# Optimization experiments

Hardware: AMD Instinct MI355X
Metric: run time of the kernel (lower is better)

## Reference

```python
import jax, jax.numpy as jnp
import numpy as np
from jax import lax

N_PER_GRAPH = 1024
B_GRAPHS = 64
AVG_DEG = 16
IN_DIM = 128
HID = 128


def setup_inputs() -> dict:
    key = jax.random.key(0)
    ks = jax.random.split(key, 16)
    N = B_GRAPHS * N_PER_GRAPH
    E = N * AVG_DEG
    rng = np.random.default_rng(0)
    g = rng.integers(0, B_GRAPHS, size=E)
    src = g * N_PER_GRAPH + rng.integers(0, N_PER_GRAPH, size=E)
    dst = g * N_PER_GRAPH + rng.integers(0, N_PER_GRAPH, size=E)
    edge_index = jnp.asarray(np.stack([src, dst]), dtype=jnp.int32)
    batch = jnp.asarray(np.arange(N) // N_PER_GRAPH, dtype=jnp.int32)

    def glorot(k, fi, fo):
        return jax.random.normal(k, (fi, fo), jnp.float32) * (1.0 / np.sqrt(fi))

    return {
        "x": jax.random.normal(ks[0], (N, IN_DIM), jnp.float32),
        "edge_index": edge_index,
        "batch": batch,
        "W1": glorot(ks[1], IN_DIM, HID), "b1": jnp.zeros((HID,), jnp.float32),
        "pw1": jax.random.normal(ks[2], (HID,), jnp.float32),
        "W2": glorot(ks[3], HID, HID // 2), "b2": jnp.zeros((HID // 2,), jnp.float32),
        "pw2": jax.random.normal(ks[4], (HID // 2,), jnp.float32),
        "W3": glorot(ks[5], HID // 2, HID // 4), "b3": jnp.zeros((HID // 4,), jnp.float32),
        "pw3": jax.random.normal(ks[6], (HID // 4,), jnp.float32),
        "W4": glorot(ks[7], HID // 4, HID // 8), "b4": jnp.zeros((HID // 8,), jnp.float32),
        "linW": glorot(ks[8], HID // 8, 1), "linb": jnp.zeros((1,), jnp.float32),
    }


def gcn_conv(x, W, b, src, dst, emask):
    N = x.shape[0]
    h = x @ W                                   # [N, out]
    m = emask.astype(x.dtype)                   # [E]
    deg = jnp.ones((N,), x.dtype).at[dst].add(m)  # in-degree incl. self loop
    dis = lax.rsqrt(deg)
    coef = dis[src] * dis[dst] * m              # [E]
    agg = jnp.zeros_like(h).at[dst].add(h[src] * coef[:, None])
    return agg + h * (dis * dis)[:, None] + b   # self-loop norm = deg^-1


def topk_pool(x, pw, src, dst, emask, n):
    # PyG TopKPooling (ratio=0.5): score = tanh(x.w/||w||); keep top n//2 per graph.
    N = x.shape[0]
    B = N // n
    k = n // 2
    score = jnp.tanh((x @ pw) / jnp.linalg.norm(pw))          # [N]
    vals, idx = lax.top_k(score.reshape(B, n), k)             # per-graph top-k
    perm = (idx + jnp.arange(B)[:, None] * n).reshape(-1)     # global kept ids
    x_new = x[perm] * vals.reshape(-1, 1)
    new_id = jnp.full((N,), -1, jnp.int32).at[perm].set(jnp.arange(B * k, dtype=jnp.int32))
    ns, nd = new_id[src], new_id[dst]
    em = emask & (ns >= 0) & (nd >= 0)
    return x_new, jnp.where(em, ns, 0), jnp.where(em, nd, 0), em, k


def reference(x, edge_index, batch, W1, b1, pw1, W2, b2, pw2, W3, b3, pw3, W4, b4, linW, linb):
    src, dst = edge_index[0], edge_index[1]
    emask = jnp.ones(src.shape, bool)
    n = N_PER_GRAPH
    act = jax.nn.relu

    x = act(gcn_conv(x, W1, b1, src, dst, emask))
    x, src, dst, emask, n = topk_pool(x, pw1, src, dst, emask, n)
    x = act(gcn_conv(x, W2, b2, src, dst, emask))
    x, src, dst, emask, n = topk_pool(x, pw2, src, dst, emask, n)
    x = act(gcn_conv(x, W3, b3, src, dst, emask))
    x, src, dst, emask, n = topk_pool(x, pw3, src, dst, emask, n)
    x = act(gcn_conv(x, W4, b4, src, dst, emask))
    # global mean pool per graph (equal-sized graphs -> reshape mean)
    B = x.shape[0] // n
    xg = x.reshape(B, n, -1).mean(axis=1)                     # [B, HID//8]
    out = (xg @ linW + linb)[:, 0] * 100.0                    # [B]
    return out
```

## Files before the change

### kernel.cpp

```cpp
#include <hip/hip_runtime.h>
#include <cstdint>
#include <cstddef>

#define CAP 64
#define EC  20480
static constexpr int BG = 64;

__global__ __launch_bounds__(256) void k_scatter(const int* __restrict__ src,
                                                 const int* __restrict__ dst,
                                                 int* __restrict__ gcur,
                                                 int2* __restrict__ ebuf) {
    __shared__ int lcnt[64], lbase[64], lpos[64];
    int tid = threadIdx.x;
    if (tid < 64) { lcnt[tid] = 0; lpos[tid] = 0; }
    __syncthreads();
    int e0 = (int)blockIdx.x * 1024;
    int ss[4], dd[4], gg[4];
    #pragma unroll
    for (int i = 0; i < 4; ++i) {
        int e = e0 + i * 256 + tid;
        ss[i] = src[e]; dd[i] = dst[e];
        gg[i] = dd[i] >> 10;
        atomicAdd(&lcnt[gg[i]], 1);
    }
    __syncthreads();
    if (tid < 64) lbase[tid] = atomicAdd(&gcur[tid], lcnt[tid]);
    __syncthreads();
    #pragma unroll
    for (int i = 0; i < 4; ++i) {
        int p = atomicAdd(&lpos[gg[i]], 1);
        int pos = lbase[gg[i]] + p;
        if (pos < EC) ebuf[(size_t)gg[i] * EC + pos] = make_int2(ss[i], dd[i]);
    }
}

__global__ __launch_bounds__(1024) void k_build(const int2* __restrict__ ebuf,
                                                const int* __restrict__ gcur,
                                                int* __restrict__ cnt,
                                                float* __restrict__ dis,
                                                int* __restrict__ slots) {
    __shared__ int lc[1024];
    int g = (int)blockIdx.x, tid = (int)threadIdx.x;
    lc[tid] = 0;
    __syncthreads();
    int ec = gcur[g]; if (ec > EC) ec = EC;
    const int2* eb = &ebuf[(size_t)g * EC];
    for (int e = tid; e < ec; e += 1024) {
        int2 sd = eb[e];
        int d = sd.y & 1023;
        int pos = atomicAdd(&lc[d], 1);
        if (pos < CAP) slots[(size_t)(g * 1024 + d) * CAP + pos] = sd.x;
    }
    __syncthreads();
    int c = lc[tid];
    cnt[g * 1024 + tid] = c;
    dis[g * 1024 + tid] = rsqrtf((float)(c + 1));
}

template<int K, int OUT>
__global__ __launch_bounds__(512) void k_gemm2(const float* __restrict__ x,
                                               const float* __restrict__ W,
                                               float* __restrict__ h, int N) {
    constexpr int KT = 32;
    constexpr int RB = 128;
    constexpr int CC = OUT / 64;
    constexpr int NW4 = (KT * OUT / 4) / 512;
    __shared__ float Ws[KT * OUT];
    __shared__ float xs[KT * RB];
    int tid = (int)threadIdx.x;
    int tx = tid & 15;
    int ty = tid >> 4;
    int row0 = (int)blockIdx.x * RB;
    const float4* W4 = (const float4*)W;

    float acc[4][CC * 4];
    #pragma unroll
    for (int r = 0; r < 4; ++r)
        #pragma unroll
        for (int c = 0; c < CC * 4; ++c) acc[r][c] = 0.f;

    int xr  = tid & 127;
    int xcb = tid >> 7;

    for (int kt = 0; kt < K; kt += KT) {
        #pragma unroll
        for (int i = 0; i < NW4; ++i) {
            int idx = tid + i * 512;
            ((float4*)Ws)[idx] = W4[(size_t)kt * (OUT / 4) + idx];
        }
        const float4* xrow = (const float4*)(x + (size_t)(row0 + xr) * K + kt);
        #pragma unroll
        for (int i = 0; i < 2; ++i) {
            int c8 = xcb * 2 + i;
            float4 v = xrow[c8];
            xs[(c8 * 4 + 0) * RB + xr] = v.x;
            xs[(c8 * 4 + 1) * RB + xr] = v.y;
            xs[(c8 * 4 + 2) * RB + xr] = v.z;
            xs[(c8 * 4 + 3) * RB + xr] = v.w;
        }
        __syncthreads();
        #pragma unroll 8
        for (int k = 0; k < KT; ++k) {
            float4 av = *(const float4*)&xs[k * RB + 4 * ty];
            float4 b0 = *(const float4*)&Ws[k * OUT + 4 * tx];
            float a_[4] = {av.x, av.y, av.z, av.w};
            float b_[4] = {b0.x, b0.y, b0.z, b0.w};
            #pragma unroll
            for (int r = 0; r < 4; ++r)
                #pragma unroll
                for (int c = 0; c < 4; ++c)
                    acc[r][c] += a_[r] * b_[c];
            if constexpr (CC == 2) {
                float4 b1 = *(const float4*)&Ws[k * OUT + 64 + 4 * tx];
                float b2_[4] = {b1.x, b1.y, b1.z, b1.w};
                #pragma unroll
                for (int r = 0; r < 4; ++r)
                    #pragma unroll
                    for (int c = 0; c < 4; ++c)
                        acc[r][4 + c] += a_[r] * b2_[c];
            }
        }
        __syncthreads();
    }
    float4* h4 = (float4*)h;
    #pragma unroll
    for (int rr = 0; rr < 4; ++rr) {
        int row = row0 + 4 * ty + rr;
        float4 o0;
        o0.x = acc[rr][0]; o0.y = acc[rr][1]; o0.z = acc[rr][2]; o0.w = acc[rr][3];
        h4[(size_t)row * (OUT / 4) + tx] = o0;
        if constexpr (CC == 2) {
            float4 o1;
            o1.x = acc[rr][4]; o1.y = acc[rr][5]; o1.z = acc[rr][6]; o1.w = acc[rr][7];
            h4[(size_t)row * (OUT / 4) + 16 + tx] = o1;
        }
    }
}

template<int K, int OUT>
__global__ __launch_bounds__(256) void k_gemm(const float* __restrict__ x,
                                              const float* __restrict__ W,
                                              float* __restrict__ h, int N) {
    constexpr int ROWS = 64;
    constexpr int KT   = (K >= 64) ? 64 : K;
    constexpr int CT   = OUT / 4;
    constexpr int RT   = 256 / CT;
    constexpr int RPT  = ROWS / RT;
    constexpr int XP   = ROWS + 4;
    __shared__ float Ws[KT * OUT];
    __shared__ float xs[KT * XP];
    int tid  = threadIdx.x;
    int row0 = blockIdx.x * ROWS;
    int c    = tid % CT;
    int rt   = tid / CT;
    float acc[RPT][4];
    for (int r = 0; r < RPT; ++r)
        for (int j = 0; j < 4; ++j) acc[r][j] = 0.f;

    for (int kt = 0; kt < K; kt += KT) {
        for (int i = tid; i < KT * OUT; i += 256)
            Ws[i] = W[(size_t)(kt + i / OUT) * OUT + (i % OUT)];
        for (int i = tid; i < ROWS * KT; i += 256) {
            int r = i / KT, k = i % KT;
            xs[k * XP + r] = x[(size_t)(row0 + r) * K + kt + k];
        }
        __syncthreads();
        for (int k = 0; k < KT; ++k) {
            float4 wv = *(const float4*)&Ws[k * OUT + 4 * c];
            const float* xk = &xs[k * XP + rt * RPT];
            #pragma unroll
            for (int r = 0; r < RPT; ++r) {
                float xv = xk[r];
                acc[r][0] += xv * wv.x;
                acc[r][1] += xv * wv.y;
                acc[r][2] += xv * wv.z;
                acc[r][3] += xv * wv.w;
            }
        }
        __syncthreads();
    }
    for (int r = 0; r < RPT; ++r) {
        int row = row0 + rt * RPT + r;
        float4 o;
        o.x = acc[r][0]; o.y = acc[r][1]; o.z = acc[r][2]; o.w = acc[r][3];
        *(float4*)&h[(size_t)row * OUT + 4 * c] = o;
    }
}

template<int OUT>
__global__ __launch_bounds__(256) void k_combine4(const float* __restrict__ h,
                                                  const int* __restrict__ cnt,
                                                  const float* __restrict__ dis,
                                                  const int* __restrict__ slots,
                                                  const float* __restrict__ b,
                                                  float* __restrict__ out, int nblocks) {
    constexpr int TPN = OUT / 4;
    constexpr int NPB = 256 / TPN;
    constexpr int S4  = OUT / 4;
    int bid = (int)blockIdx.x;
    int wb  = (bid & 7) * (nblocks >> 3) + (bid >> 3);
    int i   = wb * NPB + (int)threadIdx.x / TPN;
    int fq  = (int)threadIdx.x % TPN;
    const float4* h4 = (const float4*)h;
    int ci = cnt[i];
    float di = dis[i];
    int c = ci > CAP ? CAP : ci;
    float4 hv = h4[(size_t)i * S4 + fq];
    float4 bv = *(const float4*)(b + 4 * fq);
    float4 acc;
    acc.x = hv.x * di * di + bv.x;
    acc.y = hv.y * di * di + bv.y;
    acc.z = hv.z * di * di + bv.z;
    acc.w = hv.w * di * di + bv.w;
    const int* sl = &slots[(size_t)i * CAP];
    int j = 0;
    for (; j + 8 <= c; j += 8) {
        int4 sa = *(const int4*)(sl + j);
        int4 sb = *(const int4*)(sl + j + 4);
        float c0 = dis[sa.x] * di, c1 = dis[sa.y] * di;
        float c2 = dis[sa.z] * di, c3 = dis[sa.w] * di;
        float c4 = dis[sb.x] * di, c5 = dis[sb.y] * di;
        float c6 = dis[sb.z] * di, c7 = dis[sb.w] * di;
        float4 v0 = h4[(size_t)sa.x * S4 + fq];
        float4 v1 = h4[(size_t)sa.y * S4 + fq];
        float4 v2 = h4[(size_t)sa.z * S4 + fq];
        float4 v3 = h4[(size_t)sa.w * S4 + fq];
        float4 v4 = h4[(size_t)sb.x * S4 + fq];
        float4 v5 = h4[(size_t)sb.y * S4 + fq];
        float4 v6 = h4[(size_t)sb.z * S4 + fq];
        float4 v7 = h4[(size_t)sb.w * S4 + fq];
        acc.x += v0.x * c0; acc.y += v0.y * c0; acc.z += v0.z * c0; acc.w += v0.w * c0;
        acc.x += v1.x * c1; acc.y += v1.y * c1; acc.z += v1.z * c1; acc.w += v1.w * c1;
        acc.x += v2.x * c2; acc.y += v2.y * c2; acc.z += v2.z * c2; acc.w += v2.w * c2;
        acc.x += v3.x * c3; acc.y += v3.y * c3; acc.z += v3.z * c3; acc.w += v3.w * c3;
        acc.x += v4.x * c4; acc.y += v4.y * c4; acc.z += v4.z * c4; acc.w += v4.w * c4;
        acc.x += v5.x * c5; acc.y += v5.y * c5; acc.z += v5.z * c5; acc.w += v5.w * c5;
        acc.x += v6.x * c6; acc.y += v6.y * c6; acc.z += v6.z * c6; acc.w += v6.w * c6;
        acc.x += v7.x * c7; acc.y += v7.y * c7; acc.z += v7.z * c7; acc.w += v7.w * c7;
    }
    for (; j + 4 <= c; j += 4) {
        int4 s4 = *(const int4*)(sl + j);
        float c0 = dis[s4.x] * di, c1 = dis[s4.y] * di;
        float c2 = dis[s4.z] * di, c3 = dis[s4.w] * di;
        float4 v0 = h4[(size_t)s4.x * S4 + fq];
        float4 v1 = h4[(size_t)s4.y * S4 + fq];
        float4 v2 = h4[(size_t)s4.z * S4 + fq];
        float4 v3 = h4[(size_t)s4.w * S4 + fq];
        acc.x += v0.x * c0; acc.y += v0.y * c0; acc.z += v0.z * c0; acc.w += v0.w * c0;
        acc.x += v1.x * c1; acc.y += v1.y * c1; acc.z += v1.z * c1; acc.w += v1.w * c1;
        acc.x += v2.x * c2; acc.y += v2.y * c2; acc.z += v2.z * c2; acc.w += v2.w * c2;
        acc.x += v3.x * c3; acc.y += v3.y * c3; acc.z += v3.z * c3; acc.w += v3.w * c3;
    }
    for (; j < c; ++j) {
        int s = sl[j];
        float co = dis[s] * di;
        float4 v = h4[(size_t)s * S4 + fq];
        acc.x += v.x * co; acc.y += v.y * co; acc.z += v.z * co; acc.w += v.w * co;
    }
    float4 o;
    o.x = fmaxf(acc.x, 0.f);
    o.y = fmaxf(acc.y, 0.f);
    o.z = fmaxf(acc.z, 0.f);
    o.w = fmaxf(acc.w, 0.f);
    ((float4*)out)[(size_t)i * S4 + fq] = o;
}

template<int DIM>
__global__ void k_score(const float* __restrict__ x, const float* __restrict__ pw,
                        float* __restrict__ score, int N) {
    int wave = threadIdx.x >> 6;
    int lane = threadIdx.x & 63;
    int node = blockIdx.x * (blockDim.x >> 6) + wave;
    if (node >= N) return;
    float sd = 0.f, sn = 0.f;
    for (int k = lane; k < DIM; k += 64) {
        float w = pw[k];
        sd += x[(size_t)node * DIM + k] * w;
        sn += w * w;
    }
    #pragma unroll
    for (int off = 32; off > 0; off >>= 1) {
        sd += __shfl_down(sd, off);
        sn += __shfl_down(sn, off);
    }
    if (lane == 0) score[node] = tanhf(sd * rsqrtf(sn));
}

template<int n>
__global__ void k_topk_sort(const float* __restrict__ score,
                            float* __restrict__ kvals, int* __restrict__ kperm,
                            int* __restrict__ newid) {
    constexpr int k = n / 2;
    __shared__ float ss[n];
    __shared__ int   si[n];
    int g = blockIdx.x;
    int t = threadIdx.x;
    for (int i = t; i < n; i += n / 2) {
        ss[i] = score[g * n + i];
        si[i] = i;
        newid[g * n + i] = -1;
    }
    for (int size = 2; size <= n; size <<= 1) {
        for (int stride = size >> 1; stride > 0; stride >>= 1) {
            __syncthreads();
            int lo = 2 * t - (t & (stride - 1));
            int hi = lo + stride;
            float sa = ss[lo], sb = ss[hi];
            int   ia = si[lo], ib = si[hi];
            bool aFirst = (sa > sb) || (sa == sb && ia < ib);
            bool desc = ((lo & size) == 0);
            if (desc ? !aFirst : aFirst) {
                ss[lo] = sb; ss[hi] = sa;
                si[lo] = ib; si[hi] = ia;
            }
        }
    }
    __syncthreads();
    for (int r = t; r < k; r += n / 2) {
        newid[g * n + si[r]] = g * k + r;
        kperm[g * k + r] = g * n + si[r];
        kvals[g * k + r] = ss[r];
    }
}

template<int DIM>
__global__ __launch_bounds__(256) void k_pool_post(const float* __restrict__ x,
                                                   const int* __restrict__ kperm,
                                                   const float* __restrict__ kvals,
                                                   const int* __restrict__ newid,
                                                   const int* __restrict__ cnt_old,
                                                   const int* __restrict__ slots_old,
                                                   float* __restrict__ xnew,
                                                   int* __restrict__ cnt_new,
                                                   float* __restrict__ dis_new,
                                                   int* __restrict__ slots_new,
                                                   int Nnew) {
    constexpr int S4  = DIM / 4;
    constexpr int RPB = 32;
    int r = (int)blockIdx.x * RPB + (int)threadIdx.x / 8;
    int q = (int)threadIdx.x % 8;
    if (r >= Nnew) return;
    int old = kperm[r];
    float s = kvals[r];
    const float4* x4 = (const float4*)x;
    float4* o4 = (float4*)xnew;
    #pragma unroll
    for (int it = 0; it < (S4 + 7) / 8; ++it) {
        int idx = it * 8 + q;
        if (S4 % 8 == 0 || idx < S4) {
            float4 v = x4[(size_t)old * S4 + idx];
            float4 o;
            o.x = v.x * s; o.y = v.y * s; o.z = v.z * s; o.w = v.w * s;
            o4[(size_t)r * S4 + idx] = o;
        }
    }
    if (q == 0) {
        int c = cnt_old[old];
        if (c > CAP) c = CAP;
        const int* sl = &slots_old[(size_t)old * CAP];
        int w = 0;
        for (int j = 0; j < c; ++j) {
            int ns = newid[sl[j]];
            if (ns >= 0) slots_new[(size_t)r * CAP + (w++)] = ns;
        }
        cnt_new[r] = w;
        dis_new[r] = rsqrtf((float)(w + 1));
    }
}

__global__ void k_final(const float* __restrict__ x, const float* __restrict__ linW,
                        const float* __restrict__ linb, float* __restrict__ out) {
    int g = blockIdx.x;
    int t = threadIdx.x;
    const float* xr = &x[(size_t)(g * 128 + t) * 16];
    float p = 0.f;
    #pragma unroll
    for (int f = 0; f < 16; ++f) p += xr[f] * linW[f];
    #pragma unroll
    for (int off = 32; off > 0; off >>= 1) p += __shfl_down(p, off);
    __shared__ float wsum[2];
    if ((t & 63) == 0) wsum[t >> 6] = p;
    __syncthreads();
    if (t == 0) out[g] = ((wsum[0] + wsum[1]) * (1.f / 128.f) + linb[0]) * 100.f;
}

extern "C" void kernel_launch(void* const* d_in, const int* in_sizes, int n_in,
                              void* d_out, int out_size, void* d_ws, size_t ws_size,
                              hipStream_t stream) {
    const float* x0  = (const float*)d_in[0];
    const int*   ei  = (const int*)d_in[1];
    const int    E   = in_sizes[1] / 2;
    const int    N0  = in_sizes[0] / 128;
    const float* W1  = (const float*)d_in[3];
    const float* b1  = (const float*)d_in[4];
    const float* pw1 = (const float*)d_in[5];
    const float* W2  = (const float*)d_in[6];
    const float* b2  = (const float*)d_in[7];
    const float* pw2 = (const float*)d_in[8];
    const float* W3  = (const float*)d_in[9];
    const float* b3  = (const float*)d_in[10];
    const float* pw3 = (const float*)d_in[11];
    const float* W4  = (const float*)d_in[12];
    const float* b4  = (const float*)d_in[13];
    const float* linW = (const float*)d_in[14];
    const float* linb = (const float*)d_in[15];

    char* ws = (char*)d_ws;
    size_t off = 0;
    float* A      = (float*)(ws + off); off += (size_t)N0 * 128 * 4;
    float* H      = (float*)(ws + off); off += (size_t)N0 * 128 * 4;
    float* Bb     = (float*)(ws + off); off += (size_t)(N0 / 2) * 128 * 4;
    int*   slotsA = (int*)(ws + off);   off += (size_t)N0 * CAP * 4;
    int*   slotsB = (int*)(ws + off);   off += (size_t)(N0 / 2) * CAP * 4;
    int2*  ebuf   = (int2*)(ws + off);  off += (size_t)BG * EC * 8;
    int*   cntA   = (int*)(ws + off);   off += (size_t)N0 * 4;
    int*   cntB   = (int*)(ws + off);   off += (size_t)(N0 / 2) * 4;
    float* disA   = (float*)(ws + off); off += (size_t)N0 * 4;
    float* disB   = (float*)(ws + off); off += (size_t)(N0 / 2) * 4;
    float* score  = (float*)(ws + off); off += (size_t)N0 * 4;
    int*   newid  = (int*)(ws + off);   off += (size_t)N0 * 4;
    int*   kperm  = (int*)(ws + off);   off += (size_t)(N0 / 2) * 4;
    float* kvals  = (float*)(ws + off); off += (size_t)(N0 / 2) * 4;
    int*   gcur   = (int*)(ws + off);   off += 64 * 4;

    const int* src0 = ei;
    const int* dst0 = ei + E;

    const int N1 = N0 / 2;
    const int N2 = N1 / 2;
    const int N3 = N2 / 2;

    hipMemsetAsync(gcur, 0, 64 * 4, stream);
    k_scatter<<<E / 1024, 256, 0, stream>>>(src0, dst0, gcur, ebuf);
    k_build<<<BG, 1024, 0, stream>>>(ebuf, gcur, cntA, disA, slotsA);

    k_gemm2<128, 128><<<N0 / 128, 512, 0, stream>>>(x0, W1, H, N0);
    k_combine4<128><<<N0 / 8, 256, 0, stream>>>(H, cntA, disA, slotsA, b1, A, N0 / 8);

    k_score<128><<<N0 / 4, 256, 0, stream>>>(A, pw1, score, N0);
    k_topk_sort<1024><<<BG, 512, 0, stream>>>(score, kvals, kperm, newid);
    k_pool_post<128><<<N1 / 32, 256, 0, stream>>>(A, kperm, kvals, newid,
                                                  cntA, slotsA, Bb, cntB, disB, slotsB, N1);

    k_gemm2<128, 64><<<N1 / 128, 512, 0, stream>>>(Bb, W2, H, N1);
    k_combine4<64><<<N1 / 16, 256, 0, stream>>>(H, cntB, disB, slotsB, b2, A, N1 / 16);

    k_score<64><<<N1 / 4, 256, 0, stream>>>(A, pw2, score, N1);
    k_topk_sort<512><<<BG, 256, 0, stream>>>(score, kvals, kperm, newid);
    k_pool_post<64><<<N2 / 32, 256, 0, stream>>>(A, kperm, kvals, newid,
                                                 cntB, slotsB, Bb, cntA, disA, slotsA, N2);

    k_gemm<64, 32><<<N2 / 64, 256, 0, stream>>>(Bb, W3, H, N2);
    k_combine4<32><<<N2 / 32, 256, 0, stream>>>(H, cntA, disA, slotsA, b3, A, N2 / 32);

    k_score<32><<<N2 / 4, 256, 0, stream>>>(A, pw3, score, N2);
    k_topk_sort<256><<<BG, 128, 0, stream>>>(score, kvals, kperm, newid);
    k_pool_post<32><<<N3 / 32, 256, 0, stream>>>(A, kperm, kvals, newid,
                                                 cntA, slotsA, Bb, cntB, disB, slotsB, N3);

    k_gemm<32, 16><<<N3 / 64, 256, 0, stream>>>(Bb, W4, H, N3);
    k_combine4<16><<<N3 / 64, 256, 0, stream>>>(H, cntB, disB, slotsB, b4, A, N3 / 64);

    k_final<<<BG, 128, 0, stream>>>(A, linW, linb, (float*)d_out);
}
```

Baseline: 346.6 us.

## Stage per-graph feature slices in LDS for first-layer GCN aggregation

Replaces the first-layer combine kernel with one that loads a 32-feature slice of all 1024 node rows of a graph into shared memory (144 KB padded), then gathers neighbour rows from LDS instead of global memory. Each block covers one graph and one quarter of the feature columns. The aim is to turn random global gathers into LDS reads. The cost is a very large LDS footprint, so only one block fits per CU and only 256 blocks run in total, which may lower occupancy and parallelism.

```diff
diff --git a/kernel.cpp b/kernel.cpp
--- a/kernel.cpp
+++ b/kernel.cpp
@@ -184,6 +184,72 @@
         float4 o;
         o.x = acc[r][0]; o.y = acc[r][1]; o.z = acc[r][2]; o.w = acc[r][3];
         *(float4*)&h[(size_t)row * OUT + 4 * c] = o;
+    }
+}
+
+__global__ __launch_bounds__(1024) void k_combine_lds1(const float* __restrict__ h,
+                                                       const int* __restrict__ cnt,
+                                                       const float* __restrict__ dis,
+                                                       const int* __restrict__ slots,
+                                                       const float* __restrict__ b,
+                                                       float* __restrict__ out) {
+    constexpr int PADF = 36;
+    __shared__ float hs[1024 * PADF];
+    int bid = (int)blockIdx.x;
+    int g   = bid >> 2;
+    int ch  = bid & 3;
+    int tid = (int)threadIdx.x;
+    int jj  = tid & 7;
+    int rr  = tid >> 3;
+    const float4* h4 = (const float4*)h;
+    #pragma unroll
+    for (int p = 0; p < 8; ++p) {
+        int r = p * 128 + rr;
+        float4 v = h4[(size_t)(g * 1024 + r) * 32 + ch * 8 + jj];
+        *(float4*)&hs[r * PADF + jj * 4] = v;
+    }
+    float4 bv = ((const float4*)b)[ch * 8 + jj];
+    __syncthreads();
+    #pragma unroll 1
+    for (int p = 0; p < 8; ++p) {
+        int dl = p * 128 + rr;
+        int d  = g * 1024 + dl;
+        int ci = cnt[d];
+        float di = dis[d];
+        int c = ci > CAP ? CAP : ci;
+        const int* sl = &slots[(size_t)d * CAP];
+        float4 hv = *(const float4*)&hs[dl * PADF + jj * 4];
+        float4 acc;
+        acc.x = hv.x * di * di + bv.x;
+        acc.y = hv.y * di * di + bv.y;
+        acc.z = hv.z * di * di + bv.z;
+        acc.w = hv.w * di * di + bv.w;
+        int j = 0;
+        for (; j + 4 <= c; j += 4) {
+            int4 s4 = *(const int4*)(sl + j);
+            float c0 = dis[s4.x] * di, c1 = dis[s4.y] * di;
+            float c2 = dis[s4.z] * di, c3 = dis[s4.w] * di;
+            const float4 v0 = *(const float4*)&hs[(s4.x & 1023) * PADF + jj * 4];
+            const float4 v1 = *(const float4*)&hs[(s4.y & 1023) * PADF + jj * 4];
+            const float4 v2 = *(const float4*)&hs[(s4.z & 1023) * PADF + jj * 4];
+            const float4 v3 = *(const float4*)&hs[(s4.w & 1023) * PADF + jj * 4];
+            acc.x += v0.x * c0; acc.y += v0.y * c0; acc.z += v0.z * c0; acc.w += v0.w * c0;
+            acc.x += v1.x * c1; acc.y += v1.y * c1; acc.z += v1.z * c1; acc.w += v1.w * c1;
+            acc.x += v2.x * c2; acc.y += v2.y * c2; acc.z += v2.z * c2; acc.w += v2.w * c2;
+            acc.x += v3.x * c3; acc.y += v3.y * c3; acc.z += v3.z * c3; acc.w += v3.w * c3;
+        }
+        for (; j < c; ++j) {
+            int s = sl[j];
+            float co = dis[s] * di;
+            const float4 v = *(const float4*)&hs[(s & 1023) * PADF + jj * 4];
+            acc.x += v.x * co; acc.y += v.y * co; acc.z += v.z * co; acc.w += v.w * co;
+        }
+        float4 o;
+        o.x = fmaxf(acc.x, 0.f);
+        o.y = fmaxf(acc.y, 0.f);
+        o.z = fmaxf(acc.z, 0.f);
+        o.w = fmaxf(acc.w, 0.f);
+        ((float4*)out)[(size_t)d * 32 + ch * 8 + jj] = o;
     }
 }
 
@@ -435,7 +501,7 @@
     k_build<<<BG, 1024, 0, stream>>>(ebuf, gcur, cntA, disA, slotsA);
 
     k_gemm2<128, 128><<<N0 / 128, 512, 0, stream>>>(x0, W1, H, N0);
-    k_combine4<128><<<N0 / 8, 256, 0, stream>>>(H, cntA, disA, slotsA, b1, A, N0 / 8);
+    k_combine_lds1<<<BG * 4, 1024, 0, stream>>>(H, cntA, disA, slotsA, b1, A);
 
     k_score<128><<<N0 / 4, 256, 0, stream>>>(A, pw1, score, N0);
     k_topk_sort<1024><<<BG, 512, 0, stream>>>(score, kvals, kperm, newid);
```

After: 349.8 us. Within noise of the previous version (+0.9%).

## Fuse pool gather into GEMM and edge remap into top-k sort

Applied to the files above, without the earlier changes.

Removes the separate k_pool_post kernels. The GEMMs now gather the kept rows through kperm and scale them by kvals as they load x, so the pooled feature buffer is no longer written. The edge-list remapping moves into the top-k sort kernel, which uses a block-local new-id table in shared memory in place of a global newid array. This saves three launches and a round trip of pooled features through memory, but the slot rewrite now runs in only 64 blocks with one thread per kept node, so that step has less parallelism.

```diff
diff --git a/kernel.cpp b/kernel.cpp
--- a/kernel.cpp
+++ b/kernel.cpp
@@ -57,10 +57,12 @@
     dis[g * 1024 + tid] = rsqrtf((float)(c + 1));
 }
 
-template<int K, int OUT>
+template<int K, int OUT, bool G>
 __global__ __launch_bounds__(512) void k_gemm2(const float* __restrict__ x,
                                                const float* __restrict__ W,
-                                               float* __restrict__ h, int N) {
+                                               const int* __restrict__ kperm,
+                                               const float* __restrict__ kvals,
+                                               float* __restrict__ h) {
     constexpr int KT = 32;
     constexpr int RB = 128;
     constexpr int CC = OUT / 64;
@@ -81,6 +83,11 @@
 
     int xr  = tid & 127;
     int xcb = tid >> 7;
+    int srow = row0 + xr;
+    int orow; float sc = 1.f;
+    if constexpr (G) { orow = kperm[srow]; sc = kvals[srow]; }
+    else             { orow = srow; }
+    const float* xbase = x + (size_t)orow * K;
 
     for (int kt = 0; kt < K; kt += KT) {
         #pragma unroll
@@ -88,11 +95,12 @@
             int idx = tid + i * 512;
             ((float4*)Ws)[idx] = W4[(size_t)kt * (OUT / 4) + idx];
         }
-        const float4* xrow = (const float4*)(x + (size_t)(row0 + xr) * K + kt);
+        const float4* xrow = (const float4*)(xbase + kt);
         #pragma unroll
         for (int i = 0; i < 2; ++i) {
             int c8 = xcb * 2 + i;
             float4 v = xrow[c8];
+            if constexpr (G) { v.x *= sc; v.y *= sc; v.z *= sc; v.w *= sc; }
             xs[(c8 * 4 + 0) * RB + xr] = v.x;
             xs[(c8 * 4 + 1) * RB + xr] = v.y;
             xs[(c8 * 4 + 2) * RB + xr] = v.z;
@@ -137,10 +145,12 @@
     }
 }
 
-template<int K, int OUT>
+template<int K, int OUT, bool G>
 __global__ __launch_bounds__(256) void k_gemm(const float* __restrict__ x,
                                               const float* __restrict__ W,
-                                              float* __restrict__ h, int N) {
+                                              const int* __restrict__ kperm,
+                                              const float* __restrict__ kvals,
+                                              float* __restrict__ h) {
     constexpr int ROWS = 64;
     constexpr int KT   = (K >= 64) ? 64 : K;
     constexpr int CT   = OUT / 4;
@@ -161,8 +171,13 @@
         for (int i = tid; i < KT * OUT; i += 256)
             Ws[i] = W[(size_t)(kt + i / OUT) * OUT + (i % OUT)];
         for (int i = tid; i < ROWS * KT; i += 256) {
-            int r = i / KT, k = i % KT;
-            xs[k * XP + r] = x[(size_t)(row0 + r) * K + kt + k];
+            int r = i / KT, k2 = i % KT;
+            int sr = row0 + r;
+            if constexpr (G) {
+                xs[k2 * XP + r] = x[(size_t)kperm[sr] * K + kt + k2] * kvals[sr];
+            } else {
+                xs[k2 * XP + r] = x[(size_t)sr * K + kt + k2];
+            }
         }
         __syncthreads();
         for (int k = 0; k < KT; ++k) {
@@ -287,18 +302,22 @@
 }
 
 template<int n>
-__global__ void k_topk_sort(const float* __restrict__ score,
-                            float* __restrict__ kvals, int* __restrict__ kperm,
-                            int* __restrict__ newid) {
+__global__ void k_topk_sort2(const float* __restrict__ score,
+                             const int* __restrict__ cnt_old,
+                             const int* __restrict__ slots_old,
+                             float* __restrict__ kvals, int* __restrict__ kperm,
+                             int* __restrict__ cnt_new, float* __restrict__ dis_new,
+                             int* __restrict__ slots_new) {
     constexpr int k = n / 2;
     __shared__ float ss[n];
     __shared__ int   si[n];
+    __shared__ int   nl[n];
     int g = blockIdx.x;
     int t = threadIdx.x;
-    for (int i = t; i < n; i += n / 2) {
+    for (int i = t; i < n; i += k) {
         ss[i] = score[g * n + i];
         si[i] = i;
-        newid[g * n + i] = -1;
+        nl[i] = -1;
     }
     for (int size = 2; size <= n; size <<= 1) {
         for (int stride = size >> 1; stride > 0; stride >>= 1) {
@@ -316,55 +335,25 @@
         }
     }
     __syncthreads();
-    for (int r = t; r < k; r += n / 2) {
-        newid[g * n + si[r]] = g * k + r;
-        kperm[g * k + r] = g * n + si[r];
-        kvals[g * k + r] = ss[r];
-    }
-}
-
-template<int DIM>
-__global__ __launch_bounds__(256) void k_pool_post(const float* __restrict__ x,
-                                                   const int* __restrict__ kperm,
-                                                   const float* __restrict__ kvals,
-                                                   const int* __restrict__ newid,
-                                                   const int* __restrict__ cnt_old,
-                                                   const int* __restrict__ slots_old,
-                                                   float* __restrict__ xnew,
-                                                   int* __restrict__ cnt_new,
-                                                   float* __restrict__ dis_new,
-                                                   int* __restrict__ slots_new,
-                                                   int Nnew) {
-    constexpr int S4  = DIM / 4;
-    constexpr int RPB = 32;
-    int r = (int)blockIdx.x * RPB + (int)threadIdx.x / 8;
-    int q = (int)threadIdx.x % 8;
-    if (r >= Nnew) return;
-    int old = kperm[r];
-    float s = kvals[r];
-    const float4* x4 = (const float4*)x;
-    float4* o4 = (float4*)xnew;
-    #pragma unroll
-    for (int it = 0; it < (S4 + 7) / 8; ++it) {
-        int idx = it * 8 + q;
-        if (S4 % 8 == 0 || idx < S4) {
-            float4 v = x4[(size_t)old * S4 + idx];
-            float4 o;
-            o.x = v.x * s; o.y = v.y * s; o.z = v.z * s; o.w = v.w * s;
-            o4[(size_t)r * S4 + idx] = o;
-        }
-    }
-    if (q == 0) {
+    {
+        nl[si[t]] = g * k + t;
+        kperm[g * k + t] = g * n + si[t];
+        kvals[g * k + t] = ss[t];
+    }
+    __syncthreads();
+    {
+        int old = g * n + si[t];
         int c = cnt_old[old];
         if (c > CAP) c = CAP;
         const int* sl = &slots_old[(size_t)old * CAP];
+        int* sn = &slots_new[(size_t)(g * k + t) * CAP];
         int w = 0;
         for (int j = 0; j < c; ++j) {
-            int ns = newid[sl[j]];
-            if (ns >= 0) slots_new[(size_t)r * CAP + (w++)] = ns;
-        }
-        cnt_new[r] = w;
-        dis_new[r] = rsqrtf((float)(w + 1));
+            int ns = nl[sl[j] - g * n];
+            if (ns >= 0) sn[w++] = ns;
+        }
+        cnt_new[g * k + t] = w;
+        dis_new[g * k + t] = rsqrtf((float)(w + 1));
     }
 }
 
@@ -409,7 +398,6 @@
     size_t off = 0;
     float* A      = (float*)(ws + off); off += (size_t)N0 * 128 * 4;
     float* H      = (float*)(ws + off); off += (size_t)N0 * 128 * 4;
-    float* Bb     = (float*)(ws + off); off += (size_t)(N0 / 2) * 128 * 4;
     int*   slotsA = (int*)(ws + off);   off += (size_t)N0 * CAP * 4;
     int*   slotsB = (int*)(ws + off);   off += (size_t)(N0 / 2) * CAP * 4;
     int2*  ebuf   = (int2*)(ws + off);  off += (size_t)BG * EC * 8;
@@ -418,7 +406,6 @@
     float* disA   = (float*)(ws + off); off += (size_t)N0 * 4;
     float* disB   = (float*)(ws + off); off += (size_t)(N0 / 2) * 4;
     float* score  = (float*)(ws + off); off += (size_t)N0 * 4;
-    int*   newid  = (int*)(ws + off);   off += (size_t)N0 * 4;
     int*   kperm  = (int*)(ws + off);   off += (size_t)(N0 / 2) * 4;
     float* kvals  = (float*)(ws + off); off += (size_t)(N0 / 2) * 4;
     int*   gcur   = (int*)(ws + off);   off += 64 * 4;
@@ -434,31 +421,28 @@
     k_scatter<<<E / 1024, 256, 0, stream>>>(src0, dst0, gcur, ebuf);
     k_build<<<BG, 1024, 0, stream>>>(ebuf, gcur, cntA, disA, slotsA);
 
-    k_gemm2<128, 128><<<N0 / 128, 512, 0, stream>>>(x0, W1, H, N0);
+    k_gemm2<128, 128, false><<<N0 / 128, 512, 0, stream>>>(x0, W1, nullptr, nullptr, H);
     k_combine4<128><<<N0 / 8, 256, 0, stream>>>(H, cntA, disA, slotsA, b1, A, N0 / 8);
 
     k_score<128><<<N0 / 4, 256, 0, stream>>>(A, pw1, score, N0);
-    k_topk_sort<1024><<<BG, 512, 0, stream>>>(score, kvals, kperm, newid);
-    k_pool_post<128><<<N1 / 32, 256, 0, stream>>>(A, kperm, kvals, newid,
-                                                  cntA, slotsA, Bb, cntB, disB, slotsB, N1);
-
-    k_gemm2<128, 64><<<N1 / 128, 512, 0, stream>>>(Bb, W2, H, N1);
+    k_topk_sort2<1024><<<BG, 512, 0, stream>>>(score, cntA, slotsA,
+                                               kvals, kperm, cntB, disB, slotsB);
+
+    k_gemm2<128, 64, true><<<N1 / 128, 512, 0, stream>>>(A, W2, kperm, kvals, H);
     k_combine4<64><<<N1 / 16, 256, 0, stream>>>(H, cntB, disB, slotsB, b2, A, N1 / 16);
 
     k_score<64><<<N1 / 4, 256, 0, stream>>>(A, pw2, score, N1);
-    k_topk_sort<512><<<BG, 256, 0, stream>>>(score, kvals, kperm, newid);
-    k_pool_post<64><<<N2 / 32, 256, 0, stream>>>(A, kperm, kvals, newid,
-                                                 cntB, slotsB, Bb, cntA, disA, slotsA, N2);
-
-    k_gemm<64, 32><<<N2 / 64, 256, 0, stream>>>(Bb, W3, H, N2);
+    k_topk_sort2<512><<<BG, 256, 0, stream>>>(score, cntB, slotsB,
+                                              kvals, kperm, cntA, disA, slotsA);
+
+    k_gemm<64, 32, true><<<N2 / 64, 256, 0, stream>>>(A, W3, kperm, kvals, H);
     k_combine4<32><<<N2 / 32, 256, 0, stream>>>(H, cntA, disA, slotsA, b3, A, N2 / 32);
 
     k_score<32><<<N2 / 4, 256, 0, stream>>>(A, pw3, score, N2);
-    k_topk_sort<256><<<BG, 128, 0, stream>>>(score, kvals, kperm, newid);
-    k_pool_post<32><<<N3 / 32, 256, 0, stream>>>(A, kperm, kvals, newid,
-                                                 cntA, slotsA, Bb, cntB, disB, slotsB, N3);
-
-    k_gemm<32, 16><<<N3 / 64, 256, 0, stream>>>(Bb, W4, H, N3);
+    k_topk_sort2<256><<<BG, 128, 0, stream>>>(score, cntA, slotsA,
+                                              kvals, kperm, cntB, disB, slotsB);
+
+    k_gemm<32, 16, true><<<N3 / 64, 256, 0, stream>>>(A, W4, kperm, kvals, H);
     k_combine4<16><<<N3 / 64, 256, 0, stream>>>(H, cntB, disB, slotsB, b4, A, N3 / 64);
 
     k_final<<<BG, 128, 0, stream>>>(A, linW, linb, (float*)d_out);
```

New measurement: 336.5 us. 2.9% less time.
